# Kernel optimization log

Hardware: AMD Instinct MI355X
Metric: run time of the kernel (lower is better)

Reference implementation:

```python
import jax, jax.numpy as jnp
import numpy as np


def _min_euclid_block(x, sh):
    # x: [B, C, T], sh: [C, K, S]
    S = sh.shape[-1]
    T = x.shape[2]
    W = T - S + 1  # number of sliding windows
    idx = jnp.arange(W)[:, None] + jnp.arange(S)[None, :]  # [W, S]
    xu = x[:, :, idx]  # [B, C, W, S] sliding windows (unfold)
    # pairwise euclidean distance via the Gram expansion (same math as cdist)
    x2 = jnp.sum(xu * xu, axis=-1)          # [B, C, W]
    s2 = jnp.sum(sh * sh, axis=-1)          # [C, K]
    xs = jnp.einsum('bcws,cks->bcwk', xu, sh)  # [B, C, W, K]
    d2 = x2[..., None] + s2[None, :, None, :] - 2.0 * xs
    d = jnp.sqrt(jnp.maximum(d2, 1e-12))    # [B, C, W, K]
    d = jnp.sum(d, axis=1, keepdims=True)   # sum over channels -> [B, 1, W, K]
    return jnp.min(d, axis=2)               # min over windows -> [B, 1, K]


def setup_inputs() -> dict:
    key = jax.random.key(0)
    k0, k1, k2, k3 = jax.random.split(key, 4)
    B, C, T, K = 32, 3, 2048, 128
    return {
        'x': jax.random.normal(k0, (B, C, T), dtype=jnp.float32),
        'sh16': jax.random.normal(k1, (C, K, 16), dtype=jnp.float32),
        'sh32': jax.random.normal(k2, (C, K, 32), dtype=jnp.float32),
        'sh64': jax.random.normal(k3, (C, K, 64), dtype=jnp.float32),
    }


def reference(x, sh16, sh32, sh64):
    # ShapeletsDistBlocks with dist_measure='euclidean': run each
    # MinEuclideanDistBlock and concatenate along the shapelet axis (dim 2).
    outs = [_min_euclid_block(x, sh) for sh in (sh16, sh32, sh64)]
    return jnp.concatenate(outs, axis=2)  # [B, 1, sum(K)]
```

## Files before the change

kernel.cpp:

```cpp
#include <hip/hip_runtime.h>

typedef __attribute__((ext_vector_type(8)))  __bf16 bf16x8;
typedef __attribute__((ext_vector_type(16))) float  f32x16;

#define DEV __device__ __forceinline__

namespace {

constexpr int BB = 32, CC = 3, TT = 2048, KK = 128, OUTK = 384;
constexpr int TP = 2176;

constexpr size_t OFF_B16 = 0;
constexpr size_t OFF_B32 = 12288;
constexpr size_t OFF_B64 = 36864;
constexpr size_t OFF_S2  = 86016;
constexpr size_t OFF_X2  = 90624;
constexpr size_t OFF_XC  = 2449920;

DEV unsigned short rne(float f) {
  unsigned u = __float_as_uint(f);
  u += 0x7FFFu + ((u >> 16) & 1u);
  return (unsigned short)(u >> 16);
}
DEV float rnef(float f) {
  unsigned u = __float_as_uint(f);
  u += 0x7FFFu + ((u >> 16) & 1u);
  return __uint_as_float(u & 0xFFFF0000u);
}
DEV uint4 pack8(const unsigned short* h) {
  uint4 d;
  d.x = (unsigned)h[0] | ((unsigned)h[1] << 16);
  d.y = (unsigned)h[2] | ((unsigned)h[3] << 16);
  d.z = (unsigned)h[4] | ((unsigned)h[5] << 16);
  d.w = (unsigned)h[6] | ((unsigned)h[7] << 16);
  return d;
}
DEV float f4get(const float4 v, int j) {
  switch (j) { case 0: return v.x; case 1: return v.y; case 2: return v.z; default: return v.w; }
}

constexpr int N_OUT = BB * OUTK;
constexpr int N_BF  = 5376;
constexpr int N_S2  = 1152;
constexpr int N_XC  = BB * CC * 8 * (TP/8);
constexpr int N_X2  = BB * CC * TT;
constexpr int N_TOT = N_OUT + N_BF + N_S2 + N_XC + N_X2;

__global__ __launch_bounds__(256) void precompute(
    const float* __restrict__ x, const float* __restrict__ sh16,
    const float* __restrict__ sh32, const float* __restrict__ sh64,
    unsigned char* __restrict__ ws, unsigned* __restrict__ outu)
{
  int i = blockIdx.x * 256 + threadIdx.x;
  if (i >= N_TOT) return;
  if (i < N_OUT) { outu[i] = 0x7f800000u; return; }
  i -= N_OUT;

  if (i < N_BF) {
    int S, it; const float* sh; size_t boff;
    if (i < 768)       { S = 16; it = i;        sh = sh16; boff = OFF_B16; }
    else if (i < 2304) { S = 32; it = i - 768;  sh = sh32; boff = OFF_B32; }
    else               { S = 64; it = i - 2304; sh = sh64; boff = OFF_B64; }
    const int CHS = S / 8, KST = S / 16;
    int c = it / (KK * CHS); int r = it - c * KK * CHS;
    int n = r / CHS;         int k0 = (r - n * CHS) * 8;
    const float* src = sh + ((size_t)(c * KK + n)) * S + k0;
    unsigned short h[8];
    #pragma unroll
    for (int j = 0; j < 8; ++j) h[j] = rne(src[j]);
    ((uint4*)(ws + boff))[((c * 4 + (n >> 5)) * KST + (k0 >> 4)) * 64 + ((k0 >> 3) & 1) * 32 + (n & 31)] = pack8(h);
    return;
  }
  i -= N_BF;

  if (i < N_S2) {
    int Sidx = i / 384; int r = i - Sidx * 384; int c = r >> 7; int k = r & 127;
    int S = 16 << Sidx;
    const float* sh = (Sidx == 0) ? sh16 : ((Sidx == 1) ? sh32 : sh64);
    const float* sp = sh + ((size_t)(c * KK + k)) * S;
    float acc = 0.f;
    #pragma unroll 4
    for (int s = 0; s < S; ++s) { float v = rnef(sp[s]); acc = fmaf(v, v, acc); }
    ((float*)(ws + OFF_S2))[(Sidx * CC + c) * KK + k] = acc;
    return;
  }
  i -= N_S2;

  if (i < N_XC) {
    const int per = TP / 8;
    int c8 = i / per; int q8 = i - c8 * per;
    int p  = c8 & 7;  int bc = c8 >> 3;
    const float* xb = x + (size_t)bc * TT;
    int m0 = q8 * 8;
    unsigned short h[8];
    #pragma unroll
    for (int j = 0; j < 8; ++j) {
      int mi = m0 + j + p;
      float v = (mi < TT) ? xb[mi] : 0.f;
      h[j] = rne(v);
    }
    ((uint4*)(ws + OFF_XC + (size_t)c8 * TP * 2))[q8] = pack8(h);
    return;
  }
  i -= N_XC;

  {
    int w = i & (TT - 1); int bc = i >> 11;
    const float* xb = x + (size_t)bc * TT;
    float acc = 0.f, a16, a32, a64;
    #pragma unroll 4
    for (int s = 0; s < 16; ++s) { int mi = w + s; float v = (mi < TT) ? rnef(xb[mi]) : 0.f; acc = fmaf(v, v, acc); }
    a16 = acc;
    #pragma unroll 4
    for (int s = 16; s < 32; ++s) { int mi = w + s; float v = (mi < TT) ? rnef(xb[mi]) : 0.f; acc = fmaf(v, v, acc); }
    a32 = acc;
    #pragma unroll 4
    for (int s = 32; s < 64; ++s) { int mi = w + s; float v = (mi < TT) ? rnef(xb[mi]) : 0.f; acc = fmaf(v, v, acc); }
    a64 = acc;
    float* x2 = (float*)(ws + OFF_X2);
    x2[(size_t)(0 * BB * CC + bc) * TT + w] = a16;
    x2[(size_t)(1 * BB * CC + bc) * TT + w] = a32;
    x2[(size_t)(2 * BB * CC + bc) * TT + w] = a64;
  }
}

template<int KST> struct Frag { uint4 A[KST]; uint4 B[KST]; };

template<int KST>
DEV void issueAB(const unsigned short* __restrict__ xA, const uint4* __restrict__ bB, Frag<KST>& F) {
  #pragma unroll
  for (int kk = 0; kk < KST; ++kk) {
    F.A[kk] = *(const uint4*)(xA + 16 * kk);
    F.B[kk] = bB[kk * 64];
  }
}
template<int KST>
DEV f32x16 domfma(const Frag<KST>& F) {
  f32x16 a{};
  #pragma unroll
  for (int kk = 0; kk < KST; ++kk)
    a = __builtin_amdgcn_mfma_f32_32x32x16_bf16(
        __builtin_bit_cast(bf16x8, F.A[kk]), __builtin_bit_cast(bf16x8, F.B[kk]), a, 0, 0, 0);
  return a;
}
DEV void epi(const f32x16 a, const float* __restrict__ x2c, float s2c, int lhi, f32x16& dsum) {
  #pragma unroll
  for (int g = 0; g < 4; ++g) {
    const float4 xq = *(const float4*)(x2c + 4 * lhi + 8 * g);
    #pragma unroll
    for (int j = 0; j < 4; ++j) {
      const int r2 = g * 4 + j;
      dsum[r2] += __builtin_amdgcn_sqrtf(fmaxf(fmaf(-2.f, a[r2], f4get(xq, j) + s2c), 1e-12f));
    }
  }
}

template<int S, int KST, int OUTOFF, size_t BOFF, int SIDX>
DEV void run(const unsigned char* __restrict__ ws, unsigned* __restrict__ outu,
             int r, float* __restrict__ x2l, float* __restrict__ s2l)
{
  const int b = r >> 6, t = r & 63, wblk = t >> 1, kblk = t & 1;
  const int tid = (int)threadIdx.x;
  const int lane = tid & 63;
  const int l31 = lane & 31, lhi = lane >> 5, p = l31 & 7;
  const int wsub = (tid >> 6) & 1, ksub = tid >> 7;
  const int w0 = wblk * 64 + wsub * 32;
  const int kq = kblk * 2 + ksub;

  const float* x2g = (const float*)(ws + OFF_X2) + (size_t)(SIDX * BB * CC + b * CC) * TT;
  const float* s2g = (const float*)(ws + OFF_S2) + SIDX * CC * KK;
  if (tid < 192) {
    int c = tid >> 6, w = tid & 63;
    x2l[tid] = x2g[(size_t)c * TT + wblk * 64 + w];
    s2l[tid] = s2g[c * KK + kblk * 64 + w];
  }
  __syncthreads();

  const unsigned short* xA = (const unsigned short*)(ws + OFF_XC)
      + ((size_t)(b * CC * 8) + p) * TP + (w0 + 8 * (l31 >> 3) + 8 * lhi);
  const uint4* bB = (const uint4*)(ws + BOFF) + (size_t)(kq * KST) * 64 + lane;

  Frag<KST> F0, F1, F2;
  issueAB<KST>(xA, bB, F0);
  issueAB<KST>(xA + 8 * TP, bB + 4 * KST * 64, F1);

  f32x16 dsum{};
  const float* x2w = x2l + wsub * 32;
  const float s20 = s2l[0 * 64 + ksub * 32 + l31];
  const float s21 = s2l[1 * 64 + ksub * 32 + l31];
  const float s22 = s2l[2 * 64 + ksub * 32 + l31];

  f32x16 a0 = domfma<KST>(F0);
  issueAB<KST>(xA + 16 * TP, bB + 8 * KST * 64, F2);
  epi(a0, x2w + 0 * 64, s20, lhi, dsum);
  f32x16 a1 = domfma<KST>(F1);
  epi(a1, x2w + 1 * 64, s21, lhi, dsum);
  f32x16 a2 = domfma<KST>(F2);
  epi(a2, x2w + 2 * 64, s22, lhi, dsum);

  constexpr int W = TT - S + 1;
  float m = __builtin_inff();
  if (w0 + 31 < W) {
    #pragma unroll
    for (int r2 = 0; r2 < 16; ++r2) m = fminf(m, dsum[r2]);
  } else {
    #pragma unroll
    for (int r2 = 0; r2 < 16; ++r2) {
      const int ro = (r2 & 3) + 8 * (r2 >> 2) + 4 * lhi;
      if (w0 + ro < W) m = fminf(m, dsum[r2]);
    }
  }
  m = fminf(m, __shfl_xor(m, 32));
  if (lane < 32)
    atomicMin(outu + (b * OUTK + OUTOFF + kq * 32 + l31), __float_as_uint(m));
}

__global__ __launch_bounds__(256, 2) void shapelets_main(
    const unsigned char* __restrict__ ws, unsigned* __restrict__ outu)
{
  __shared__ __attribute__((aligned(16))) float x2l[192];
  __shared__ __attribute__((aligned(16))) float s2l[192];
  const int j = (int)blockIdx.x;
  if (j < 2048)      run<16, 1,   0, OFF_B16, 0>(ws, outu, j,        x2l, s2l);
  else if (j < 4096) run<32, 2, 128, OFF_B32, 1>(ws, outu, j - 2048, x2l, s2l);
  else               run<64, 4, 256, OFF_B64, 2>(ws, outu, j - 4096, x2l, s2l);
}

}

extern "C" void kernel_launch(void* const* d_in, const int* in_sizes, int n_in,
                              void* d_out, int out_size, void* d_ws, size_t ws_size,
                              hipStream_t stream) {
  const float* x    = (const float*)d_in[0];
  const float* sh16 = (const float*)d_in[1];
  const float* sh32 = (const float*)d_in[2];
  const float* sh64 = (const float*)d_in[3];
  unsigned* outu = (unsigned*)d_out;
  unsigned char* ws = (unsigned char*)d_ws;

  precompute<<<(N_TOT + 255) / 256, 256, 0, stream>>>(x, sh16, sh32, sh64, ws, outu);
  shapelets_main<<<6144, 256, 0, stream>>>(ws, outu);
}
```

Measured before the change: 47.64 us.

## Reuse x window fragments across all shapelet quarters per block

Each block now covers 128 windows and all 128 shapelets of one batch, with 4 waves splitting the windows. A fragments are loaded once per channel and reused across four shapelet quarters, with B fragments streamed per quarter. The grid drops from 6144 to 1536 blocks, and launch bounds rise to 3 blocks per CU. The goal is fewer redundant A loads and less per-block setup overhead. The cost is less cross-stage prefetch overlap, more serial work per wave, and possible register pressure under the new launch bound.

```diff
diff --git a/kernel.cpp b/kernel.cpp
--- a/kernel.cpp
+++ b/kernel.cpp
@@ -124,25 +124,6 @@
   }
 }
 
-template<int KST> struct Frag { uint4 A[KST]; uint4 B[KST]; };
-
-template<int KST>
-DEV void issueAB(const unsigned short* __restrict__ xA, const uint4* __restrict__ bB, Frag<KST>& F) {
-  #pragma unroll
-  for (int kk = 0; kk < KST; ++kk) {
-    F.A[kk] = *(const uint4*)(xA + 16 * kk);
-    F.B[kk] = bB[kk * 64];
-  }
-}
-template<int KST>
-DEV f32x16 domfma(const Frag<KST>& F) {
-  f32x16 a{};
-  #pragma unroll
-  for (int kk = 0; kk < KST; ++kk)
-    a = __builtin_amdgcn_mfma_f32_32x32x16_bf16(
-        __builtin_bit_cast(bf16x8, F.A[kk]), __builtin_bit_cast(bf16x8, F.B[kk]), a, 0, 0, 0);
-  return a;
-}
 DEV void epi(const f32x16 a, const float* __restrict__ x2c, float s2c, int lhi, f32x16& dsum) {
   #pragma unroll
   for (int g = 0; g < 4; ++g) {
@@ -159,71 +140,81 @@
 DEV void run(const unsigned char* __restrict__ ws, unsigned* __restrict__ outu,
              int r, float* __restrict__ x2l, float* __restrict__ s2l)
 {
-  const int b = r >> 6, t = r & 63, wblk = t >> 1, kblk = t & 1;
+  const int b = r >> 4, wg = r & 15;
   const int tid = (int)threadIdx.x;
-  const int lane = tid & 63;
+  const int lane = tid & 63, wsub = tid >> 6;
   const int l31 = lane & 31, lhi = lane >> 5, p = l31 & 7;
-  const int wsub = (tid >> 6) & 1, ksub = tid >> 7;
-  const int w0 = wblk * 64 + wsub * 32;
-  const int kq = kblk * 2 + ksub;
-
-  const float* x2g = (const float*)(ws + OFF_X2) + (size_t)(SIDX * BB * CC + b * CC) * TT;
+  const int w0 = wg * 128 + wsub * 32;
+
+  const float* x2g = (const float*)(ws + OFF_X2) + (size_t)(SIDX * BB * CC + b * CC) * TT + wg * 128;
   const float* s2g = (const float*)(ws + OFF_S2) + SIDX * CC * KK;
-  if (tid < 192) {
-    int c = tid >> 6, w = tid & 63;
-    x2l[tid] = x2g[(size_t)c * TT + wblk * 64 + w];
-    s2l[tid] = s2g[c * KK + kblk * 64 + w];
+  #pragma unroll
+  for (int i0 = 0; i0 < 2; ++i0) {
+    int i = i0 * 256 + tid;
+    if (i < 384) {
+      int c = i >> 7, q = i & 127;
+      x2l[i] = x2g[(size_t)c * TT + q];
+      s2l[i] = s2g[c * KK + q];
+    }
   }
   __syncthreads();
 
-  const unsigned short* xA = (const unsigned short*)(ws + OFF_XC)
-      + ((size_t)(b * CC * 8) + p) * TP + (w0 + 8 * (l31 >> 3) + 8 * lhi);
-  const uint4* bB = (const uint4*)(ws + BOFF) + (size_t)(kq * KST) * 64 + lane;
-
-  Frag<KST> F0, F1, F2;
-  issueAB<KST>(xA, bB, F0);
-  issueAB<KST>(xA + 8 * TP, bB + 4 * KST * 64, F1);
-
-  f32x16 dsum{};
-  const float* x2w = x2l + wsub * 32;
-  const float s20 = s2l[0 * 64 + ksub * 32 + l31];
-  const float s21 = s2l[1 * 64 + ksub * 32 + l31];
-  const float s22 = s2l[2 * 64 + ksub * 32 + l31];
-
-  f32x16 a0 = domfma<KST>(F0);
-  issueAB<KST>(xA + 16 * TP, bB + 8 * KST * 64, F2);
-  epi(a0, x2w + 0 * 64, s20, lhi, dsum);
-  f32x16 a1 = domfma<KST>(F1);
-  epi(a1, x2w + 1 * 64, s21, lhi, dsum);
-  f32x16 a2 = domfma<KST>(F2);
-  epi(a2, x2w + 2 * 64, s22, lhi, dsum);
-
+  const unsigned short* XCb = (const unsigned short*)(ws + OFF_XC);
+  uint4 A[CC][KST];
+  #pragma unroll
+  for (int c = 0; c < CC; ++c) {
+    const unsigned short* xA = XCb + ((size_t)((b * CC + c) * 8) + p) * TP
+                             + (w0 + 8 * (l31 >> 3) + 8 * lhi);
+    #pragma unroll
+    for (int kk = 0; kk < KST; ++kk) A[c][kk] = *(const uint4*)(xA + 16 * kk);
+  }
+
+  const uint4* Bg = (const uint4*)(ws + BOFF) + lane;
   constexpr int W = TT - S + 1;
-  float m = __builtin_inff();
-  if (w0 + 31 < W) {
-    #pragma unroll
-    for (int r2 = 0; r2 < 16; ++r2) m = fminf(m, dsum[r2]);
-  } else {
-    #pragma unroll
-    for (int r2 = 0; r2 < 16; ++r2) {
-      const int ro = (r2 & 3) + 8 * (r2 >> 2) + 4 * lhi;
-      if (w0 + ro < W) m = fminf(m, dsum[r2]);
-    }
-  }
-  m = fminf(m, __shfl_xor(m, 32));
-  if (lane < 32)
-    atomicMin(outu + (b * OUTK + OUTOFF + kq * 32 + l31), __float_as_uint(m));
-}
-
-__global__ __launch_bounds__(256, 2) void shapelets_main(
+
+  #pragma unroll
+  for (int kq = 0; kq < 4; ++kq) {
+    f32x16 dsum{};
+    #pragma unroll
+    for (int c = 0; c < CC; ++c) {
+      uint4 Bf[KST];
+      #pragma unroll
+      for (int kk = 0; kk < KST; ++kk)
+        Bf[kk] = Bg[(size_t)(((c * 4 + kq) * KST + kk)) * 64];
+      f32x16 acc{};
+      #pragma unroll
+      for (int kk = 0; kk < KST; ++kk)
+        acc = __builtin_amdgcn_mfma_f32_32x32x16_bf16(
+            __builtin_bit_cast(bf16x8, A[c][kk]), __builtin_bit_cast(bf16x8, Bf[kk]), acc, 0, 0, 0);
+      const float s2c = s2l[c * 128 + kq * 32 + l31];
+      epi(acc, x2l + c * 128 + wsub * 32, s2c, lhi, dsum);
+    }
+    float m = __builtin_inff();
+    if (w0 + 31 < W) {
+      #pragma unroll
+      for (int r2 = 0; r2 < 16; ++r2) m = fminf(m, dsum[r2]);
+    } else {
+      #pragma unroll
+      for (int r2 = 0; r2 < 16; ++r2) {
+        const int ro = (r2 & 3) + 8 * (r2 >> 2) + 4 * lhi;
+        if (w0 + ro < W) m = fminf(m, dsum[r2]);
+      }
+    }
+    m = fminf(m, __shfl_xor(m, 32));
+    if (lane < 32)
+      atomicMin(outu + (b * OUTK + OUTOFF + kq * 32 + l31), __float_as_uint(m));
+  }
+}
+
+__global__ __launch_bounds__(256, 3) void shapelets_main(
     const unsigned char* __restrict__ ws, unsigned* __restrict__ outu)
 {
-  __shared__ __attribute__((aligned(16))) float x2l[192];
-  __shared__ __attribute__((aligned(16))) float s2l[192];
+  __shared__ __attribute__((aligned(16))) float x2l[384];
+  __shared__ __attribute__((aligned(16))) float s2l[384];
   const int j = (int)blockIdx.x;
-  if (j < 2048)      run<16, 1,   0, OFF_B16, 0>(ws, outu, j,        x2l, s2l);
-  else if (j < 4096) run<32, 2, 128, OFF_B32, 1>(ws, outu, j - 2048, x2l, s2l);
-  else               run<64, 4, 256, OFF_B64, 2>(ws, outu, j - 4096, x2l, s2l);
+  if (j < 512)       run<16, 1,   0, OFF_B16, 0>(ws, outu, j,        x2l, s2l);
+  else if (j < 1024) run<32, 2, 128, OFF_B32, 1>(ws, outu, j - 512,  x2l, s2l);
+  else               run<64, 4, 256, OFF_B64, 2>(ws, outu, j - 1024, x2l, s2l);
 }
 
 }
@@ -239,5 +230,5 @@
   unsigned char* ws = (unsigned char*)d_ws;
 
   precompute<<<(N_TOT + 255) / 256, 256, 0, stream>>>(x, sh16, sh32, sh64, ws, outu);
-  shapelets_main<<<6144, 256, 0, stream>>>(ws, outu);
-}
+  shapelets_main<<<1536, 256, 0, stream>>>(ws, outu);
+}
```

Measured after the change: 39.63 us. 16.8% less time.
